# Kernel optimization log

Hardware: AMD Instinct MI355X
Metric: run time of the kernel (lower is better)

Reference implementation:

```python
import jax, jax.numpy as jnp
import numpy as np

N_HEAD, D_K = 16, 64  # from init_kwargs (d_v == d_k)

def setup_inputs() -> dict:
    key = jax.random.key(0)
    ks = jax.random.split(key, 8)
    B, S, D, DFF = 8, 1024, 1024, 4096
    s = 1.0 / np.sqrt(D)
    return {
        "enc_input": jax.random.normal(ks[0], (B, S, D), jnp.float32),
        "mask": jnp.ones((B, 1, S), jnp.int32),
        "gap": 1,
        "wq": jax.random.normal(ks[1], (D, N_HEAD * D_K), jnp.float32) * s,
        "wk": jax.random.normal(ks[2], (D, N_HEAD * D_K), jnp.float32) * s,
        "wv": jax.random.normal(ks[3], (D, N_HEAD * D_K), jnp.float32) * s,
        "wo": jax.random.normal(ks[4], (N_HEAD * D_K, D), jnp.float32) * s,
        "w1": jax.random.normal(ks[5], (D, DFF), jnp.float32) * s,
        "b1": jnp.zeros((DFF,), jnp.float32),
        "w2": jax.random.normal(ks[6], (DFF, D), jnp.float32) * (1.0 / np.sqrt(DFF)),
        "b2": jnp.zeros((D,), jnp.float32),
    }

def reference(enc_input, mask, gap, wq, wk, wv, wo, w1, b1, w2, b2):
    # dropout=0, use_layer_norm=0, adapter=0 are hard-coded in EncoderLayer.__init__
    B, S, D = enc_input.shape
    H, dk = N_HEAD, D_K
    temperature = dk ** 0.5

    q = (enc_input @ wq).reshape(B, S, H, dk).transpose(0, 2, 1, 3)  # [B,H,S,dk]
    k = (enc_input @ wk).reshape(B, S, H, dk).transpose(0, 2, 1, 3)
    v = (enc_input @ wv).reshape(B, S, H, dk).transpose(0, 2, 1, 3)

    attn = jnp.einsum('bhqd,bhkd->bhqk', q / temperature, k)  # [B,H,S,S]
    # mask [B,1,S] -> unsqueeze head dim -> [B,1,1,S]
    attn = jnp.where(mask[:, None] == 0, jnp.float32(-1e9), attn)
    attn = jax.nn.softmax(attn, axis=-1)

    ctx = jnp.einsum('bhqk,bhkd->bhqd', attn, v)          # [B,H,S,dk]
    ctx = ctx.transpose(0, 2, 1, 3).reshape(B, S, H * dk)  # [B,S,D]
    enc = ctx @ wo + enc_input                              # attn residual

    ffn = jax.nn.relu(enc @ w1 + b1) @ w2 + b2
    out = ffn + enc                                         # ffn residual
    return out, attn
```

## Files before the change

### kernel.cpp

```cpp
#include <hip/hip_runtime.h>
#include <hip/hip_bf16.h>
#include <stdint.h>

typedef __bf16 bf16x8 __attribute__((ext_vector_type(8)));
typedef float  f32x4  __attribute__((ext_vector_type(4)));

typedef __attribute__((address_space(1))) void gvoid;
typedef __attribute__((address_space(3))) void lvoid;

__device__ __forceinline__ void async16(void* lds, const void* g) {
    __builtin_amdgcn_global_load_lds((gvoid*)g, (lvoid*)lds, 16, 0, 0);
}

__device__ __forceinline__ float fexp2(float x) {
    return __builtin_amdgcn_exp2f(x);
}

__global__ void prep_all(const float* __restrict__ X, __hip_bfloat16* __restrict__ Xb,
                         const float* __restrict__ wq, const float* __restrict__ wk,
                         const float* __restrict__ wv, const float* __restrict__ wo,
                         const float* __restrict__ w1, const float* __restrict__ w2,
                         __hip_bfloat16* __restrict__ Wcat,
                         __hip_bfloat16* __restrict__ Wot,
                         __hip_bfloat16* __restrict__ W1t,
                         __hip_bfloat16* __restrict__ W2t) {
    const int tix = blockIdx.x;
    if (tix >= 12288) {
        const int bi = tix - 12288;
        const int tid = threadIdx.y * 32 + threadIdx.x;
        const long i = ((long)bi * 256 + tid) * 4;
        float4 v = *(const float4*)(X + i);
        __hip_bfloat162* d = (__hip_bfloat162*)(Xb + i);
        d[0] = __float22bfloat162_rn(make_float2(v.x, v.y));
        d[1] = __float22bfloat162_rn(make_float2(v.z, v.w));
        return;
    }
    __shared__ float t[32][33];
    const float* in;
    __hip_bfloat16* out;
    int R, C, cx, cy;
    if (tix < 4096) {
        int wid = tix >> 10, tile = tix & 1023;
        const float* srcs[4] = {wq, wk, wv, wo};
        __hip_bfloat16* dsts[4] = {Wcat, Wcat + 1024 * 1024, Wcat + 2 * 1024 * 1024, Wot};
        in = srcs[wid]; out = dsts[wid];
        R = 1024; C = 1024; cx = tile & 31; cy = tile >> 5;
    } else if (tix < 8192) {
        int tile = tix - 4096;
        in = w1; out = W1t; R = 1024; C = 4096;
        cx = tile & 127; cy = tile >> 7;
    } else {
        int tile = tix - 8192;
        in = w2; out = W2t; R = 4096; C = 1024;
        cx = tile & 31; cy = tile >> 5;
    }
    const int c0 = cx * 32, r0 = cy * 32;
    const int tx = threadIdx.x, ty = threadIdx.y;
#pragma unroll
    for (int i = 0; i < 4; ++i) {
        int r = r0 + ty + i * 8;
        t[ty + i * 8][tx] = in[(long)r * C + c0 + tx];
    }
    __syncthreads();
#pragma unroll
    for (int i = 0; i < 4; ++i) {
        int c = c0 + ty + i * 8;
        out[(long)c * R + r0 + tx] = __float2bfloat16(t[tx][ty + i * 8]);
    }
}

__global__ void transpose_v(const __hip_bfloat16* __restrict__ QKV,
                            __hip_bfloat16* __restrict__ Vt) {
    __shared__ __hip_bfloat16 t[32][33];
    int s0 = blockIdx.x * 32, d0 = blockIdx.y * 32, z = blockIdx.z;
    int b = z >> 4, h = z & 15;
    int tx = threadIdx.x, ty = threadIdx.y;
#pragma unroll
    for (int i = 0; i < 4; ++i) {
        int s = s0 + ty + i * 8;
        t[ty + i * 8][tx] = QKV[((long)b * 1024 + s) * 3072 + 2048 + h * 64 + d0 + tx];
    }
    __syncthreads();
#pragma unroll
    for (int i = 0; i < 4; ++i) {
        int d = d0 + ty + i * 8;
        Vt[((long)z * 64 + d) * 1024 + s0 + tx] = t[tx][ty + i * 8];
    }
}

#define RBAR asm volatile("s_barrier" ::: "memory")

__global__ void __launch_bounds__(256, 2)
attn_fused(const __hip_bfloat16* __restrict__ QKV,
           const __hip_bfloat16* __restrict__ Vt,
           const int* __restrict__ mask,
           float* __restrict__ attn,
           __hip_bfloat16* __restrict__ Ctx) {
    __shared__ __align__(16) __hip_bfloat16 sK[128 * 64];
    __shared__ __align__(16) __hip_bfloat16 sV[64 * 128];
    __shared__ __align__(16) __hip_bfloat16 sP[128 * 128];
    __shared__ float smadd[1024];

    const int tid = threadIdx.x, lane = tid & 63, wave = tid >> 6;
    const int r16 = lane & 15, kg = lane >> 4;
    const float SC2 = 0.125f * 1.44269504f;

    const int dd = blockIdx.x;
    const int wgt = (dd & 7) * 128 + (dd >> 3);
    const int xblk = wgt & 7, z = wgt >> 3;
    const int b = z >> 4, h = z & 15;
    const int row0 = xblk * 128;
    const int wrow = wave * 32;

    const __hip_bfloat16* Qz = QKV + ((long)b * 1024 + row0) * 3072 + h * 64;
    const __hip_bfloat16* Kz = QKV + (long)b * 1024 * 3072 + 1024 + h * 64;
    const __hip_bfloat16* Vz = Vt + (long)z * 64 * 1024;
    float* attnZ = attn + (long)z * 1024 * 1024 + (long)row0 * 1024;

    for (int i = tid; i < 1024; i += 256)
        smadd[i] = mask[b * 1024 + i] ? 0.f : -1.5e9f;

    bf16x8 qa[2][2];
#pragma unroll
    for (int m = 0; m < 2; ++m)
#pragma unroll
        for (int kf = 0; kf < 2; ++kf)
            qa[m][kf] = *(const bf16x8*)(Qz + (long)(wrow + m * 16 + r16) * 3072 + kf * 32 + kg * 8);

    float lrow[2][4];
#pragma unroll
    for (int m = 0; m < 2; ++m)
#pragma unroll
        for (int i = 0; i < 4; ++i) lrow[m][i] = 0.f;

    const int ssw = (r16 & 7) << 4;

    auto stageK = [&](char* dst, int ct) {
#pragma unroll
        for (int j = 0; j < 4; ++j) {
            int c = wave * 4 + j;
            int s = c * 8 + (lane >> 3);
            int cb = (lane & 7) * 16;
            async16(dst + c * 1024,
                    (const char*)(Kz + (long)(ct * 128 + s) * 3072) + (cb ^ ((s & 7) << 4)));
        }
    };
    auto stageV = [&](int ct) {
#pragma unroll
        for (int j = 0; j < 4; ++j) {
            int c = wave * 4 + j;
            int dv = c * 4 + (lane >> 4);
            int cb = (lane & 15) * 16;
            async16((char*)sV + c * 1024,
                    (const char*)(Vz + (long)dv * 1024 + ct * 128) + (cb ^ ((dv & 7) << 4)));
        }
    };

    char* kbuf0 = (char*)sK;
    char* kbuf1 = (char*)sP;
    stageK(kbuf0, 0);

    for (int ct = 0; ct < 8; ++ct) {
        asm volatile("s_waitcnt vmcnt(0)" ::: "memory");
        __syncthreads();
        if (ct < 7) stageK((ct & 1) ? kbuf0 : kbuf1, ct + 1);
        const char* base = (ct & 1) ? kbuf1 : kbuf0;

        f32x4 sacc[2][8];
#pragma unroll
        for (int m = 0; m < 2; ++m)
#pragma unroll
            for (int nf = 0; nf < 8; ++nf) sacc[m][nf] = f32x4{0.f, 0.f, 0.f, 0.f};

        __builtin_amdgcn_s_setprio(1);
#pragma unroll
        for (int nf = 0; nf < 8; ++nf) {
            const char* kr = base + (nf * 16 + r16) * 128;
            bf16x8 bv0 = *(const bf16x8*)(kr + ((kg * 16) ^ ssw));
            bf16x8 bv1 = *(const bf16x8*)(kr + ((64 + kg * 16) ^ ssw));
#pragma unroll
            for (int m = 0; m < 2; ++m) {
                sacc[m][nf] = __builtin_amdgcn_mfma_f32_16x16x32_bf16(qa[m][0], bv0, sacc[m][nf], 0, 0, 0);
                sacc[m][nf] = __builtin_amdgcn_mfma_f32_16x16x32_bf16(qa[m][1], bv1, sacc[m][nf], 0, 0, 0);
            }
        }
        __builtin_amdgcn_s_setprio(0);

        float madd[8];
#pragma unroll
        for (int nf = 0; nf < 8; ++nf) madd[nf] = smadd[ct * 128 + nf * 16 + r16];

#pragma unroll
        for (int m = 0; m < 2; ++m)
#pragma unroll
            for (int i = 0; i < 4; ++i) {
                float ts = 0.f;
#pragma unroll
                for (int nf = 0; nf < 8; ++nf)
                    ts += fexp2(sacc[m][nf][i] * SC2 + madd[nf]);
#pragma unroll
                for (int o = 1; o < 16; o <<= 1) ts += __shfl_xor(ts, o);
                lrow[m][i] += ts;
            }
    }

    float rinv[2][4];
#pragma unroll
    for (int m = 0; m < 2; ++m)
#pragma unroll
        for (int i = 0; i < 4; ++i) rinv[m][i] = 1.0f / lrow[m][i];

    f32x4 oacc[2][4];
#pragma unroll
    for (int m = 0; m < 2; ++m)
#pragma unroll
        for (int nf = 0; nf < 4; ++nf) oacc[m][nf] = f32x4{0.f, 0.f, 0.f, 0.f};

    __syncthreads();
    stageK((char*)sK, 0);
    stageV(0);

    for (int ct = 0; ct < 8; ++ct) {
        asm volatile("s_waitcnt vmcnt(0)" ::: "memory");
        __syncthreads();

        f32x4 sacc[2][8];
#pragma unroll
        for (int m = 0; m < 2; ++m)
#pragma unroll
            for (int nf = 0; nf < 8; ++nf) sacc[m][nf] = f32x4{0.f, 0.f, 0.f, 0.f};

        __builtin_amdgcn_s_setprio(1);
#pragma unroll
        for (int nf = 0; nf < 8; ++nf) {
            const char* kr = (const char*)sK + (nf * 16 + r16) * 128;
            bf16x8 bv0 = *(const bf16x8*)(kr + ((kg * 16) ^ ssw));
            bf16x8 bv1 = *(const bf16x8*)(kr + ((64 + kg * 16) ^ ssw));
#pragma unroll
            for (int m = 0; m < 2; ++m) {
                sacc[m][nf] = __builtin_amdgcn_mfma_f32_16x16x32_bf16(qa[m][0], bv0, sacc[m][nf], 0, 0, 0);
                sacc[m][nf] = __builtin_amdgcn_mfma_f32_16x16x32_bf16(qa[m][1], bv1, sacc[m][nf], 0, 0, 0);
            }
        }
        __builtin_amdgcn_s_setprio(0);

        RBAR;
        if (ct < 7) stageK((char*)sK, ct + 1);

        float madd[8];
#pragma unroll
        for (int nf = 0; nf < 8; ++nf) madd[nf] = smadd[ct * 128 + nf * 16 + r16];

#pragma unroll
        for (int m = 0; m < 2; ++m)
#pragma unroll
            for (int nf = 0; nf < 8; ++nf) {
                int scol = nf * 16 + r16;
#pragma unroll
                for (int i = 0; i < 4; ++i) {
                    int q = wrow + m * 16 + kg * 4 + i;
                    float p = fexp2(sacc[m][nf][i] * SC2 + madd[nf]) * rinv[m][i];
                    __builtin_nontemporal_store(p, attnZ + (long)q * 1024 + ct * 128 + scol);
                    *(__hip_bfloat16*)((char*)sP + q * 256 + ((scol * 2) ^ ((q & 7) << 4))) =
                        __float2bfloat16(p);
                }
            }

        __builtin_amdgcn_s_setprio(1);
#pragma unroll
        for (int ks = 0; ks < 4; ++ks) {
            bf16x8 pa[2], vv[4];
#pragma unroll
            for (int m = 0; m < 2; ++m)
                pa[m] = *(const bf16x8*)((const char*)sP + (wrow + m * 16 + r16) * 256 +
                                         ((ks * 64 + kg * 16) ^ ssw));
#pragma unroll
            for (int nf = 0; nf < 4; ++nf)
                vv[nf] = *(const bf16x8*)((const char*)sV + (nf * 16 + r16) * 256 +
                                          ((ks * 64 + kg * 16) ^ ssw));
#pragma unroll
            for (int m = 0; m < 2; ++m)
#pragma unroll
                for (int nf = 0; nf < 4; ++nf)
                    oacc[m][nf] = __builtin_amdgcn_mfma_f32_16x16x32_bf16(pa[m], vv[nf], oacc[m][nf], 0, 0, 0);
        }
        __builtin_amdgcn_s_setprio(0);

        RBAR;
        if (ct < 7) stageV(ct + 1);
    }

#pragma unroll
    for (int m = 0; m < 2; ++m)
#pragma unroll
        for (int nf = 0; nf < 4; ++nf)
#pragma unroll
            for (int i = 0; i < 4; ++i) {
                int q = wrow + m * 16 + kg * 4 + i;
                Ctx[((long)b * 1024 + row0 + q) * 1024 + h * 64 + nf * 16 + r16] =
                    __float2bfloat16(oacc[m][nf][i]);
            }
}

#define RDA(BUF, PM, ML, KS) \
    (*(const bf16x8*)(aRd + (BUF)*32768 + (PM)*16384 + (ML)*2048 + ((((KS)*64) + kg*16) ^ sw)))
#define RDB(BUF, PN, NL, KS) \
    (*(const bf16x8*)(bRd + (BUF)*32768 + (PN)*16384 + (NL)*2048 + ((((KS)*64) + kg*16) ^ sw)))
#define LOAD_A(BUF, PM)                          \
    _Pragma("unroll") for (int ml = 0; ml < 4; ++ml) \
    _Pragma("unroll") for (int ks = 0; ks < 2; ++ks) \
        a[ml][ks] = RDA(BUF, PM, ml, ks)
#define LOAD_B(DST, BUF, PN)                     \
    _Pragma("unroll") for (int nl = 0; nl < 2; ++nl) \
    _Pragma("unroll") for (int ks = 0; ks < 2; ++ks) \
        DST[nl][ks] = RDB(BUF, PN, nl, ks)
#define MFMA16(PM, PN, BB)                                                   \
    __builtin_amdgcn_s_setprio(1);                                           \
    _Pragma("unroll") for (int ks = 0; ks < 2; ++ks)                         \
    _Pragma("unroll") for (int ml = 0; ml < 4; ++ml)                         \
    _Pragma("unroll") for (int nl = 0; nl < 2; ++nl)                         \
        acc[(PM)*4 + ml][(PN)*2 + nl] = __builtin_amdgcn_mfma_f32_16x16x32_bf16( \
            a[ml][ks], BB[nl][ks], acc[(PM)*4 + ml][(PN)*2 + nl], 0, 0, 0);  \
    __builtin_amdgcn_s_setprio(0)
#define BAR asm volatile("s_barrier" ::: "memory")

__global__ void __launch_bounds__(512, 2)
gemm256(const __hip_bfloat16* __restrict__ A, int lda,
        const __hip_bfloat16* __restrict__ Bt, int ldb,
        int K, int Mtiles,
        const float* __restrict__ bias, int relu,
        __hip_bfloat16* __restrict__ C, int ldc) {
    __shared__ __align__(16) char lds[131072];
    const int NT = K >> 6;
    const int tid = threadIdx.x, lane = tid & 63, wave = tid >> 6;
    const int r16 = lane & 15, kg = lane >> 4;
    const int wr = wave >> 2, wc = wave & 3;
    const int sw = (r16 & 7) << 4;

    const int nwg = gridDim.x;
    const int q8 = nwg >> 3, r8 = nwg & 7;
    const int xcd = blockIdx.x & 7, rest = blockIdx.x >> 3;
    const int wg = (xcd < r8 ? xcd * (q8 + 1) : r8 * (q8 + 1) + (xcd - r8) * q8) + rest;
    const int tm = wg % Mtiles, tn = wg / Mtiles;
    const long row0 = (long)tm * 256, col0 = (long)tn * 256;

    const int idx = tid >> 3;
    const int slotp = ((tid & 7) ^ (idx & 7)) * 8;
    const __hip_bfloat16* aSrc[4];
    const __hip_bfloat16* bSrc[4];
#pragma unroll
    for (int j = 0; j < 4; ++j) {
        long ar = row0 + (j & 1) * 128 + (j >> 1) * 64 + idx;
        aSrc[j] = A + ar * lda + slotp;
        long br = col0 + ((j & 1) * 2 + (tid >> 8)) * 64 + (j >> 1) * 32 + (idx & 31);
        bSrc[j] = Bt + br * ldb + slotp;
    }

    char* ldsA = lds;
    char* ldsB = lds + 65536;
    const int stDst = wave * 1024;
    auto stA = [&](int v, int j) {
        async16(ldsA + ((v & 1) << 15) + (j << 13) + stDst, aSrc[j] + (v << 6));
    };
    auto stB = [&](int v, int j) {
        async16(ldsB + ((v & 1) << 15) + (j << 13) + stDst, bSrc[j] + (v << 6));
    };

    stA(0, 0); stA(0, 1); stB(0, 0); stB(0, 1);
    stA(0, 2); stA(0, 3); stB(0, 2); stB(0, 3);
    stA(1, 0); stA(1, 1); stB(1, 0); stB(1, 1);
    asm volatile("s_waitcnt vmcnt(4)" ::: "memory");
    BAR;

    f32x4 acc[8][4] = {};
    const char* aRd = ldsA + wr * 8192 + r16 * 128;
    const char* bRd = ldsB + wc * 4096 + r16 * 128;

    for (int u = 0; u < NT; u += 2) {
        const bool more = (u + 2) < NT;
        bf16x8 a[4][2], b0[2][2], b1[2][2];

        LOAD_A(0, 0);
        LOAD_B(b0, 0, 0);
        stA(u + 1, 2); stA(u + 1, 3);
        MFMA16(0, 0, b0);
        BAR;

        LOAD_B(b1, 0, 1);
        stB(u + 1, 2); stB(u + 1, 3);
        MFMA16(0, 1, b1);
        BAR;

        LOAD_A(0, 1);
        if (more) { stA(u + 2, 0); stA(u + 2, 1); }
        MFMA16(1, 0, b0);
        BAR;

        if (more) {
            stB(u + 2, 0); stB(u + 2, 1);
            asm volatile("s_waitcnt vmcnt(4)" ::: "memory");
        } else {
            asm volatile("s_waitcnt vmcnt(0)" ::: "memory");
        }
        MFMA16(1, 1, b1);
        BAR;

        LOAD_A(1, 0);
        LOAD_B(b0, 1, 0);
        if (more) { stA(u + 2, 2); stA(u + 2, 3); }
        MFMA16(0, 0, b0);
        BAR;

        LOAD_B(b1, 1, 1);
        if (more) { stB(u + 2, 2); stB(u + 2, 3); }
        MFMA16(0, 1, b1);
        BAR;

        LOAD_A(1, 1);
        if (more) { stA(u + 3, 0); stA(u + 3, 1); }
        MFMA16(1, 0, b0);
        BAR;

        if (more) {
            stB(u + 3, 0); stB(u + 3, 1);
            asm volatile("s_waitcnt vmcnt(4)" ::: "memory");
        }
        MFMA16(1, 1, b1);
        BAR;
    }

    const long crow = row0 + wr * 128, ccol = col0 + wc * 64;
#pragma unroll
    for (int mf = 0; mf < 8; ++mf)
#pragma unroll
        for (int nf = 0; nf < 4; ++nf) {
            const long col = ccol + nf * 16 + r16;
            const float bs = bias ? bias[col] : 0.f;
#pragma unroll
            for (int i = 0; i < 4; ++i) {
                const long row = crow + mf * 16 + kg * 4 + i;
                float v = acc[mf][nf][i] + bs;
                if (relu) v = fmaxf(v, 0.f);
                C[row * (long)ldc + col] = __float2bfloat16(v);
            }
        }
}

#define RDB128(BUF, NL, KS) \
    (*(const bf16x8*)(bRd + (BUF)*16384 + (NL)*2048 + ((((KS)*64) + kg*16) ^ sw)))
#define LOAD_B128(DST, BUF)                      \
    _Pragma("unroll") for (int nl = 0; nl < 2; ++nl) \
    _Pragma("unroll") for (int ks = 0; ks < 2; ++ks) \
        DST[nl][ks] = RDB128(BUF, nl, ks)
#define MFMA16N(PM, BB)                                                      \
    __builtin_amdgcn_s_setprio(1);                                           \
    _Pragma("unroll") for (int ks = 0; ks < 2; ++ks)                         \
    _Pragma("unroll") for (int ml = 0; ml < 4; ++ml)                         \
    _Pragma("unroll") for (int nl = 0; nl < 2; ++nl)                         \
        acc[(PM)*4 + ml][nl] = __builtin_amdgcn_mfma_f32_16x16x32_bf16(      \
            a[ml][ks], BB[nl][ks], acc[(PM)*4 + ml][nl], 0, 0, 0);           \
    __builtin_amdgcn_s_setprio(0)

__global__ void __launch_bounds__(512, 2)
gemm256n128(const __hip_bfloat16* __restrict__ A, int lda,
            const __hip_bfloat16* __restrict__ Bt, int ldb,
            int K, int Mtiles,
            const float* __restrict__ bias, int relu,
            const float* __restrict__ resf,
            const __hip_bfloat16* __restrict__ resb, int ldres,
            float* __restrict__ Cf, __hip_bfloat16* __restrict__ Cb, int ldc) {
    __shared__ __align__(16) char lds[98304];
    const int NT = K >> 6;
    const int tid = threadIdx.x, lane = tid & 63, wave = tid >> 6;
    const int r16 = lane & 15, kg = lane >> 4;
    const int wr = wave >> 2, wc = wave & 3;
    const int sw = (r16 & 7) << 4;

    const int nwg = gridDim.x;
    const int q8 = nwg >> 3, r8 = nwg & 7;
    const int xcd = blockIdx.x & 7, rest = blockIdx.x >> 3;
    const int wg = (xcd < r8 ? xcd * (q8 + 1) : r8 * (q8 + 1) + (xcd - r8) * q8) + rest;
    const int tm = wg % Mtiles, tn = wg / Mtiles;
    const long row0 = (long)tm * 256, col0 = (long)tn * 128;

    const int idx = tid >> 3;
    const int slotp = ((tid & 7) ^ (idx & 7)) * 8;
    const __hip_bfloat16* aSrc[4];
    const __hip_bfloat16* bSrc[2];
#pragma unroll
    for (int j = 0; j < 4; ++j) {
        long ar = row0 + (j & 1) * 128 + (j >> 1) * 64 + idx;
        aSrc[j] = A + ar * lda + slotp;
    }
#pragma unroll
    for (int j = 0; j < 2; ++j) {
        long br = col0 + j * 64 + idx;
        bSrc[j] = Bt + br * ldb + slotp;
    }

    char* ldsA = lds;
    char* ldsB = lds + 65536;
    const int stDst = wave * 1024;
    auto stA = [&](int v, int j) {
        async16(ldsA + ((v & 1) << 15) + (j << 13) + stDst, aSrc[j] + (v << 6));
    };
    auto stB = [&](int v, int j) {
        async16(ldsB + ((v & 1) << 14) + (j << 13) + stDst, bSrc[j] + (v << 6));
    };

    stA(0, 0); stA(0, 1); stA(0, 2); stA(0, 3);
    stB(0, 0); stB(0, 1);
    stA(1, 0); stA(1, 1);
    stB(1, 0); stB(1, 1);
    asm volatile("s_waitcnt vmcnt(4)" ::: "memory");
    BAR;

    f32x4 acc[8][2] = {};
    const char* aRd = ldsA + wr * 8192 + r16 * 128;
    const char* bRd = ldsB + wc * 4096 + r16 * 128;

    for (int u = 0; u < NT; u += 2) {
        const bool more = (u + 2) < NT;
        bf16x8 a[4][2], b0[2][2], b1[2][2];

        LOAD_A(0, 0);
        LOAD_B128(b0, 0);
        stA(u + 1, 2); stA(u + 1, 3);
        MFMA16N(0, b0);
        BAR;

        LOAD_A(0, 1);
        if (more) {
            stA(u + 2, 0); stA(u + 2, 1);
            stB(u + 2, 0); stB(u + 2, 1);
            asm volatile("s_waitcnt vmcnt(4)" ::: "memory");
        } else {
            asm volatile("s_waitcnt vmcnt(0)" ::: "memory");
        }
        MFMA16N(1, b0);
        BAR;

        LOAD_A(1, 0);
        LOAD_B128(b1, 1);
        if (more) { stA(u + 2, 2); stA(u + 2, 3); }
        MFMA16N(0, b1);
        BAR;

        LOAD_A(1, 1);
        if (more) {
            stA(u + 3, 0); stA(u + 3, 1);
            stB(u + 3, 0); stB(u + 3, 1);
            asm volatile("s_waitcnt vmcnt(4)" ::: "memory");
        }
        MFMA16N(1, b1);
        BAR;
    }

    const long crow = row0 + wr * 128, ccol = col0 + wc * 32;
#pragma unroll
    for (int mf = 0; mf < 8; ++mf)
#pragma unroll
        for (int nf = 0; nf < 2; ++nf) {
            const long col = ccol + nf * 16 + r16;
            const float bs = bias ? bias[col] : 0.f;
#pragma unroll
            for (int i = 0; i < 4; ++i) {
                const long row = crow + mf * 16 + kg * 4 + i;
                float v = acc[mf][nf][i] + bs;
                if (relu) v = fmaxf(v, 0.f);
                if (resf) v += resf[row * (long)ldres + col];
                if (resb) v += __bfloat162float(resb[row * (long)ldres + col]);
                const long off = row * (long)ldc + col;
                if (Cf) Cf[off] = v;
                if (Cb) Cb[off] = __float2bfloat16(v);
            }
        }
}

extern "C" void kernel_launch(void* const* d_in, const int* in_sizes, int n_in,
                              void* d_out, int out_size, void* d_ws, size_t ws_size,
                              hipStream_t stream) {
    const int B = 8, S = 1024, D = 1024, DFF = 4096;
    const long SD = (long)B * S * D;

    const float* X  = (const float*)d_in[0];
    const int*  msk = (const int*)d_in[1];
    const float* wq = (const float*)d_in[3];
    const float* wk = (const float*)d_in[4];
    const float* wv = (const float*)d_in[5];
    const float* wo = (const float*)d_in[6];
    const float* w1 = (const float*)d_in[7];
    const float* b1 = (const float*)d_in[8];
    const float* w2 = (const float*)d_in[9];
    const float* b2 = (const float*)d_in[10];

    float* out  = (float*)d_out;
    float* attn = out + SD;

    char* ws = (char*)d_ws;
    auto alloc = [&](size_t bytes) {
        char* p = ws;
        ws += (bytes + 255) & ~(size_t)255;
        return p;
    };
    __hip_bfloat16* Xb   = (__hip_bfloat16*)alloc(SD * 2);
    __hip_bfloat16* QKVb = (__hip_bfloat16*)alloc(SD * 3 * 2);
    __hip_bfloat16* Vt   = (__hip_bfloat16*)alloc(SD * 2);
    __hip_bfloat16* Ctx  = (__hip_bfloat16*)alloc(SD * 2);
    __hip_bfloat16* EncB = (__hip_bfloat16*)alloc(SD * 2);
    __hip_bfloat16* Hb   = (__hip_bfloat16*)alloc((long)B * S * DFF * 2);
    __hip_bfloat16* Wcat = (__hip_bfloat16*)alloc((long)3 * D * D * 2);
    __hip_bfloat16* Wot  = (__hip_bfloat16*)alloc((long)D * D * 2);
    __hip_bfloat16* W1t  = (__hip_bfloat16*)alloc((long)D * DFF * 2);
    __hip_bfloat16* W2t  = (__hip_bfloat16*)alloc((long)D * DFF * 2);
    (void)ws_size; (void)in_sizes; (void)n_in; (void)out_size;

    dim3 tb(32, 8);
    prep_all<<<dim3(12288 + 8192), tb, 0, stream>>>(X, Xb, wq, wk, wv, wo, w1, w2,
                                                    Wcat, Wot, W1t, W2t);

    gemm256<<<dim3(32 * 12), 512, 0, stream>>>(
        Xb, D, Wcat, D, D, 32, nullptr, 0, QKVb, 3 * D);

    transpose_v<<<dim3(32, 2, 128), tb, 0, stream>>>(QKVb, Vt);

    attn_fused<<<dim3(1024), 256, 0, stream>>>(QKVb, Vt, msk, attn, Ctx);

    gemm256n128<<<dim3(32 * 8), 512, 0, stream>>>(
        Ctx, D, Wot, D, D, 32,
        nullptr, 0, X, nullptr, D,
        nullptr, EncB, D);

    gemm256<<<dim3(32 * 16), 512, 0, stream>>>(
        EncB, D, W1t, D, D, 32, b1, 1, Hb, DFF);

    gemm256n128<<<dim3(32 * 8), 512, 0, stream>>>(
        Hb, DFF, W2t, DFF, DFF, 32,
        b2, 0, nullptr, EncB, D,
        out, nullptr, D);
}
```

Baseline: 522.3 us.

## Fuse V projection with transpose into dedicated GEMM epilogue

Splits the QKV projection into a Q/K GEMM writing a 2048-wide buffer and a new V GEMM whose epilogue transposes its tile through LDS and writes V directly in the per-head transposed layout. This removes the separate transpose_v kernel and its extra read and write of V. The V GEMM uses 256x128 tiles, so the projection now runs as two launches of 256 blocks each instead of one launch of 384. The attention kernel's Q/K strides are updated to match.

```diff
diff --git a/kernel.cpp b/kernel.cpp
--- a/kernel.cpp
+++ b/kernel.cpp
@@ -69,29 +69,10 @@
     }
 }
 
-__global__ void transpose_v(const __hip_bfloat16* __restrict__ QKV,
-                            __hip_bfloat16* __restrict__ Vt) {
-    __shared__ __hip_bfloat16 t[32][33];
-    int s0 = blockIdx.x * 32, d0 = blockIdx.y * 32, z = blockIdx.z;
-    int b = z >> 4, h = z & 15;
-    int tx = threadIdx.x, ty = threadIdx.y;
-#pragma unroll
-    for (int i = 0; i < 4; ++i) {
-        int s = s0 + ty + i * 8;
-        t[ty + i * 8][tx] = QKV[((long)b * 1024 + s) * 3072 + 2048 + h * 64 + d0 + tx];
-    }
-    __syncthreads();
-#pragma unroll
-    for (int i = 0; i < 4; ++i) {
-        int d = d0 + ty + i * 8;
-        Vt[((long)z * 64 + d) * 1024 + s0 + tx] = t[tx][ty + i * 8];
-    }
-}
-
 #define RBAR asm volatile("s_barrier" ::: "memory")
 
 __global__ void __launch_bounds__(256, 2)
-attn_fused(const __hip_bfloat16* __restrict__ QKV,
+attn_fused(const __hip_bfloat16* __restrict__ QKb,
            const __hip_bfloat16* __restrict__ Vt,
            const int* __restrict__ mask,
            float* __restrict__ attn,
@@ -112,8 +93,8 @@
     const int row0 = xblk * 128;
     const int wrow = wave * 32;
 
-    const __hip_bfloat16* Qz = QKV + ((long)b * 1024 + row0) * 3072 + h * 64;
-    const __hip_bfloat16* Kz = QKV + (long)b * 1024 * 3072 + 1024 + h * 64;
+    const __hip_bfloat16* Qz = QKb + ((long)b * 1024 + row0) * 2048 + h * 64;
+    const __hip_bfloat16* Kz = QKb + (long)b * 1024 * 2048 + 1024 + h * 64;
     const __hip_bfloat16* Vz = Vt + (long)z * 64 * 1024;
     float* attnZ = attn + (long)z * 1024 * 1024 + (long)row0 * 1024;
 
@@ -125,7 +106,7 @@
     for (int m = 0; m < 2; ++m)
 #pragma unroll
         for (int kf = 0; kf < 2; ++kf)
-            qa[m][kf] = *(const bf16x8*)(Qz + (long)(wrow + m * 16 + r16) * 3072 + kf * 32 + kg * 8);
+            qa[m][kf] = *(const bf16x8*)(Qz + (long)(wrow + m * 16 + r16) * 2048 + kf * 32 + kg * 8);
 
     float lrow[2][4];
 #pragma unroll
@@ -142,7 +123,7 @@
             int s = c * 8 + (lane >> 3);
             int cb = (lane & 7) * 16;
             async16(dst + c * 1024,
-                    (const char*)(Kz + (long)(ct * 128 + s) * 3072) + (cb ^ ((s & 7) << 4)));
+                    (const char*)(Kz + (long)(ct * 128 + s) * 2048) + (cb ^ ((s & 7) << 4)));
         }
     };
     auto stageV = [&](int ct) {
@@ -577,6 +558,131 @@
         }
 }
 
+__global__ void __launch_bounds__(512, 2)
+gemm_v(const __hip_bfloat16* __restrict__ A, int lda,
+       const __hip_bfloat16* __restrict__ Bt, int ldb,
+       int K,
+       __hip_bfloat16* __restrict__ Vt) {
+    __shared__ __align__(16) char lds[98304];
+    const int NT = K >> 6;
+    const int tid = threadIdx.x, lane = tid & 63, wave = tid >> 6;
+    const int r16 = lane & 15, kg = lane >> 4;
+    const int wr = wave >> 2, wc = wave & 3;
+    const int sw = (r16 & 7) << 4;
+
+    const int nwg = gridDim.x;
+    const int q8 = nwg >> 3, r8 = nwg & 7;
+    const int xcd = blockIdx.x & 7, rest = blockIdx.x >> 3;
+    const int wg = (xcd < r8 ? xcd * (q8 + 1) : r8 * (q8 + 1) + (xcd - r8) * q8) + rest;
+    const int tm = wg & 31, tn = wg >> 5;
+    const long row0 = (long)tm * 256, col0 = (long)tn * 128;
+
+    const int idx = tid >> 3;
+    const int slotp = ((tid & 7) ^ (idx & 7)) * 8;
+    const __hip_bfloat16* aSrc[4];
+    const __hip_bfloat16* bSrc[2];
+#pragma unroll
+    for (int j = 0; j < 4; ++j) {
+        long ar = row0 + (j & 1) * 128 + (j >> 1) * 64 + idx;
+        aSrc[j] = A + ar * lda + slotp;
+    }
+#pragma unroll
+    for (int j = 0; j < 2; ++j) {
+        long br = col0 + j * 64 + idx;
+        bSrc[j] = Bt + br * ldb + slotp;
+    }
+
+    char* ldsA = lds;
+    char* ldsB = lds + 65536;
+    const int stDst = wave * 1024;
+    auto stA = [&](int v, int j) {
+        async16(ldsA + ((v & 1) << 15) + (j << 13) + stDst, aSrc[j] + (v << 6));
+    };
+    auto stB = [&](int v, int j) {
+        async16(ldsB + ((v & 1) << 14) + (j << 13) + stDst, bSrc[j] + (v << 6));
+    };
+
+    stA(0, 0); stA(0, 1); stA(0, 2); stA(0, 3);
+    stB(0, 0); stB(0, 1);
+    stA(1, 0); stA(1, 1);
+    stB(1, 0); stB(1, 1);
+    asm volatile("s_waitcnt vmcnt(4)" ::: "memory");
+    BAR;
+
+    f32x4 acc[8][2] = {};
+    const char* aRd = ldsA + wr * 8192 + r16 * 128;
+    const char* bRd = ldsB + wc * 4096 + r16 * 128;
+
+    for (int u = 0; u < NT; u += 2) {
+        const bool more = (u + 2) < NT;
+        bf16x8 a[4][2], b0[2][2], b1[2][2];
+
+        LOAD_A(0, 0);
+        LOAD_B128(b0, 0);
+        stA(u + 1, 2); stA(u + 1, 3);
+        MFMA16N(0, b0);
+        BAR;
+
+        LOAD_A(0, 1);
+        if (more) {
+            stA(u + 2, 0); stA(u + 2, 1);
+            stB(u + 2, 0); stB(u + 2, 1);
+            asm volatile("s_waitcnt vmcnt(4)" ::: "memory");
+        } else {
+            asm volatile("s_waitcnt vmcnt(0)" ::: "memory");
+        }
+        MFMA16N(1, b0);
+        BAR;
+
+        LOAD_A(1, 0);
+        LOAD_B128(b1, 1);
+        if (more) { stA(u + 2, 2); stA(u + 2, 3); }
+        MFMA16N(0, b1);
+        BAR;
+
+        LOAD_A(1, 1);
+        if (more) {
+            stA(u + 3, 0); stA(u + 3, 1);
+            stB(u + 3, 0); stB(u + 3, 1);
+            asm volatile("s_waitcnt vmcnt(4)" ::: "memory");
+        }
+        MFMA16N(1, b1);
+        BAR;
+    }
+
+    __hip_bfloat16* sT = (__hip_bfloat16*)lds;
+    {
+        const int cls = wc * 32;
+        const int rls = wr * 128 + kg * 4;
+#pragma unroll
+        for (int mf = 0; mf < 8; ++mf)
+#pragma unroll
+            for (int nf = 0; nf < 2; ++nf) {
+                int cl = cls + nf * 16 + r16;
+                int rl = rls + mf * 16;
+                __hip_bfloat162 lo = __float22bfloat162_rn(make_float2(acc[mf][nf][0], acc[mf][nf][1]));
+                __hip_bfloat162 hi = __float22bfloat162_rn(make_float2(acc[mf][nf][2], acc[mf][nf][3]));
+                *(__hip_bfloat162*)(&sT[cl * 264 + rl]) = lo;
+                *(__hip_bfloat162*)(&sT[cl * 264 + rl + 2]) = hi;
+            }
+    }
+    __syncthreads();
+    {
+        const int b = (int)(row0 >> 10);
+        const int s_base = (int)(row0 & 1023);
+#pragma unroll
+        for (int j = 0; j < 8; ++j) {
+            int dl = wave * 16 + j * 2 + (lane >> 5);
+            int sc = (lane & 31) * 8;
+            bf16x8 v = *(const bf16x8*)(&sT[dl * 264 + sc]);
+            int dg = (int)col0 + dl;
+            int z = b * 16 + (dg >> 6);
+            int d = dg & 63;
+            *(bf16x8*)(Vt + ((long)z * 64 + d) * 1024 + s_base + sc) = v;
+        }
+    }
+}
+
 extern "C" void kernel_launch(void* const* d_in, const int* in_sizes, int n_in,
                               void* d_out, int out_size, void* d_ws, size_t ws_size,
                               hipStream_t stream) {
@@ -604,7 +710,7 @@
         return p;
     };
     __hip_bfloat16* Xb   = (__hip_bfloat16*)alloc(SD * 2);
-    __hip_bfloat16* QKVb = (__hip_bfloat16*)alloc(SD * 3 * 2);
+    __hip_bfloat16* QKb  = (__hip_bfloat16*)alloc(SD * 4);
     __hip_bfloat16* Vt   = (__hip_bfloat16*)alloc(SD * 2);
     __hip_bfloat16* Ctx  = (__hip_bfloat16*)alloc(SD * 2);
     __hip_bfloat16* EncB = (__hip_bfloat16*)alloc(SD * 2);
@@ -619,12 +725,13 @@
     prep_all<<<dim3(12288 + 8192), tb, 0, stream>>>(X, Xb, wq, wk, wv, wo, w1, w2,
                                                     Wcat, Wot, W1t, W2t);
 
-    gemm256<<<dim3(32 * 12), 512, 0, stream>>>(
-        Xb, D, Wcat, D, D, 32, nullptr, 0, QKVb, 3 * D);
-
-    transpose_v<<<dim3(32, 2, 128), tb, 0, stream>>>(QKVb, Vt);
-
-    attn_fused<<<dim3(1024), 256, 0, stream>>>(QKVb, Vt, msk, attn, Ctx);
+    gemm256<<<dim3(32 * 8), 512, 0, stream>>>(
+        Xb, D, Wcat, D, D, 32, nullptr, 0, QKb, 2048);
+
+    gemm_v<<<dim3(32 * 8), 512, 0, stream>>>(
+        Xb, D, Wcat + (long)2048 * 1024, D, D, Vt);
+
+    attn_fused<<<dim3(1024), 256, 0, stream>>>(QKb, Vt, msk, attn, Ctx);
 
     gemm256n128<<<dim3(32 * 8), 512, 0, stream>>>(
         Ctx, D, Wot, D, D, 32,
```

New measurement: 510.4 us. -2.3%, faster.
